# Performance work log

Measured on AMD Instinct MI355X. Metric: run time of the kernel, lower is better.

Reference implementation:

```python
import jax, jax.numpy as jnp
import numpy as np

VOCAB = 50257
EXTRA = 64          # static over-approximation of num_oovs
SEQ = 1024
T_DEC = 100
E = 128
H = 160             # encoder hidden per direction; decoder hidden = 2H = 320
UNK = 3
START = 0
NEG = -1e9


def lstm_cell(x, h, c, wih, whh, bih, bhh):
    # torch gate order: i, f, g, o
    g = x @ wih.T + h @ whh.T + bih + bhh
    i, f, gg, o = jnp.split(g, 4, axis=-1)
    c = jax.nn.sigmoid(f) * c + jax.nn.sigmoid(i) * jnp.tanh(gg)
    h = jax.nn.sigmoid(o) * jnp.tanh(c)
    return h, c


def run_lstm(xs, wih, whh, bih, bhh, hdim):
    def step(carry, x):
        h, c = carry
        h, c = lstm_cell(x, h, c, wih, whh, bih, bhh)
        return (h, c), h
    init = (jnp.zeros((hdim,), xs.dtype), jnp.zeros((hdim,), xs.dtype))
    (hf, _), hs = jax.lax.scan(step, init, xs)
    return hs, hf


def setup_inputs() -> dict:
    key = jax.random.key(0)
    ks = jax.random.split(key, 20)
    rn = lambda k, shape, s: (jax.random.normal(k, shape, dtype=jnp.float32) * s)
    inp = {
        'input_ids': jax.random.randint(ks[0], (SEQ,), 0, VOCAB + EXTRA),
        'embedding': rn(ks[1], (VOCAB, E), 0.1),
        'enc_wih_f': rn(ks[2], (4 * H, E), 0.08),
        'enc_whh_f': rn(ks[3], (4 * H, H), 0.08),
        'enc_bih_f': rn(ks[4], (4 * H,), 0.05),
        'enc_bhh_f': rn(ks[5], (4 * H,), 0.05),
        'enc_wih_b': rn(ks[6], (4 * H, E), 0.08),
        'enc_whh_b': rn(ks[7], (4 * H, H), 0.08),
        'enc_bih_b': rn(ks[8], (4 * H,), 0.05),
        'enc_bhh_b': rn(ks[9], (4 * H,), 0.05),
        'dec_wih': rn(ks[10], (8 * H, E), 0.08),
        'dec_whh': rn(ks[11], (8 * H, 2 * H), 0.08),
        'dec_bih': rn(ks[12], (8 * H,), 0.05),
        'dec_bhh': rn(ks[13], (8 * H,), 0.05),
        'enc_attn_proj': rn(ks[14], (2 * H, 2 * H), 0.02),
        'dec_attn_proj': rn(ks[15], (2 * H, 2 * H), 0.02),
        'vocab_proj': rn(ks[16], (E, 6 * H), 0.05),
        'out_bias': rn(ks[17], (VOCAB,), 0.01),
        'switch_w': rn(ks[18], (1, 6 * H), 0.05),
        'switch_b': rn(ks[19], (1,), 0.05),
    }
    return inp


def reference(input_ids, embedding, enc_wih_f, enc_whh_f, enc_bih_f, enc_bhh_f,
              enc_wih_b, enc_whh_b, enc_bih_b, enc_bhh_b,
              dec_wih, dec_whh, dec_bih, dec_bhh,
              enc_attn_proj, dec_attn_proj, vocab_proj, out_bias,
              switch_w, switch_b):
    ids_in = jnp.where(input_ids >= VOCAB, UNK, input_ids)
    emb = embedding[ids_in]                               # [S, E]

    # bidirectional encoder LSTM
    h_fwd, hfin_f = run_lstm(emb, enc_wih_f, enc_whh_f, enc_bih_f, enc_bhh_f, H)
    h_bwd_rev, hfin_b = run_lstm(emb[::-1], enc_wih_b, enc_whh_b, enc_bih_b, enc_bhh_b, H)
    enc_h = jnp.concatenate([h_fwd, h_bwd_rev[::-1]], axis=-1)   # [S, 2H]

    # step-invariant vocab projection: tanh(W_emb @ vocab_proj) -> [V, 6H]
    out_proj = jnp.tanh(embedding @ vocab_proj)

    # precompute projected encoder states for attention: [S, 2H]
    enc_proj_h = enc_h @ enc_attn_proj.T

    h0 = jnp.concatenate([hfin_f, hfin_b])                # [2H]
    c0 = jnp.zeros((2 * H,), enc_h.dtype)
    dec_buf0 = jnp.zeros((T_DEC, 2 * H), enc_h.dtype)
    cum0 = jnp.zeros((SEQ,), enc_h.dtype)
    tok0 = jnp.asarray(START, dtype=input_ids.dtype)
    t_range = jnp.arange(T_DEC)

    def step(carry, t):
        h, c, cum, dec_buf, tok = carry
        x = embedding[jnp.where(tok >= VOCAB, UNK, tok)]
        h, c = lstm_cell(x, h, c, dec_wih, dec_whh, dec_bih, dec_bhh)

        # intra-temporal encoder attention
        scores = enc_proj_h @ h                           # [S] = h @ W_e @ enc_h.T
        cum_safe = jnp.where(t == 0, 1.0, cum)
        temporal = jnp.where(t == 0, scores, jnp.exp(scores) / cum_safe)
        attn = jax.nn.softmax(temporal)
        enc_ctx = attn @ enc_h                            # [2H]

        # intra-decoder attention over previous decoder hidden states
        dscores = (h @ dec_attn_proj) @ dec_buf.T         # [T_DEC]
        dmask = t_range < t
        dattn = jax.nn.softmax(jnp.where(dmask, dscores, NEG))
        dec_ctx = jnp.where(t == 0, jnp.zeros_like(h), dattn @ dec_buf)

        concat = jnp.concatenate([h, enc_ctx, dec_ctx])   # [6H]
        vocab_dist = jax.nn.softmax(out_proj @ concat + out_bias)  # [V]
        p_copy = jax.nn.sigmoid(jnp.dot(switch_w[0], concat) + switch_b[0])
        gen = jnp.pad((1.0 - p_copy) * vocab_dist, (0, EXTRA))     # [V+EXTRA]
        final = gen.at[input_ids].add(p_copy * attn)      # pointer scatter-add

        cum = cum + scores
        dec_buf = dec_buf.at[t].set(h)
        tok = jnp.argmax(final).astype(input_ids.dtype)   # greedy decode
        return (h, c, cum, dec_buf, tok), final

    _, finals = jax.lax.scan(step, (h0, c0, cum0, dec_buf0, tok0), t_range)
    return finals                                         # [T_DEC, V+EXTRA]
```

## Files before the change

kernel.cpp:

```cpp
#include <hip/hip_runtime.h>
#include <cstdint>

#define VOCAB 50257
#define VTOT  50321
#define TDEC  100
#define UNK   3
#define VPB   99

static const size_t OFF_EMB    = 0;
static const size_t OFF_WIHT_F = 131072;
static const size_t OFF_WIHT_B = 212992;
static const size_t OFF_WTE    = 294912;
static const size_t OFF_XG     = 397312;
static const size_t OFF_ENCH   = 1708032;
static const size_t OFF_EPH    = 2035712;
static const size_t OFF_DECBUF = 2363392;
static const size_t OFF_LOGITS = 2395392;
static const size_t OFF_SCORES = 2446080;
static const size_t OFF_GATES  = 2447104;
static const size_t OFF_HPAR   = 2448384;
static const size_t OFF_CPAR   = 2450944;
static const size_t OFF_DCTX   = 2456064;
static const size_t OFF_H      = 2456384;
static const size_t OFF_H0     = 2456704;
static const size_t OFF_CA     = 2457024;
static const size_t OFF_CB     = 2457344;
static const size_t OFF_CUMA   = 2457664;
static const size_t OFF_CUMB   = 2458688;
static const size_t OFF_ATTN   = 2459712;
static const size_t OFF_BM     = 2460736;
static const size_t OFF_BS     = 2461248;
static const size_t OFF_AVAL   = 2461760;
static const size_t OFF_AIDX   = 2462272;
static const size_t OFF_SCAL   = 2462784;
static const size_t OFF_SKEY   = 2462848;
static const size_t OFF_SPOS   = 2463872;
static const size_t OFF_BSTART = 2464896;
static const size_t OFF_WBF16  = 2465792;

__device__ __forceinline__ float sigmf(float x) { return 1.f / (1.f + expf(-x)); }

__device__ __forceinline__ float wsum64(float x) {
#pragma unroll
  for (int m = 1; m < 64; m <<= 1) x += __shfl_xor(x, m, 64);
  return x;
}

__device__ __forceinline__ unsigned short bf16r(float x) {
  uint32_t b = __float_as_uint(x);
  uint32_t r = (b + 0x7fffu + ((b >> 16) & 1u)) >> 16;
  return (unsigned short)r;
}

__global__ __launch_bounds__(256) void k_setup(float* __restrict__ ws, const int* __restrict__ ids,
                                               const float* __restrict__ embt, const float* __restrict__ ewf,
                                               const float* __restrict__ ewb, const float* __restrict__ eap) {
  int idx = blockIdx.x * 256 + threadIdx.x;
  if (idx < 131072) {
    int tt = idx >> 7, e = idx & 127;
    int id = ids[tt]; if (id >= VOCAB) id = UNK;
    ws[OFF_EMB + idx] = embt[(size_t)id * 128 + e];
  } else if (idx < 212992) {
    int i = idx - 131072;
    int k = i / 640, g = i - (i / 640) * 640;
    ws[OFF_WIHT_F + i] = ewf[(size_t)g * 128 + k];
  } else if (idx < 294912) {
    int i = idx - 212992;
    int k = i / 640, g = i - (i / 640) * 640;
    ws[OFF_WIHT_B + i] = ewb[(size_t)g * 128 + k];
  } else if (idx < 397312) {
    int i = idx - 294912;
    int k = i / 320, j = i - (i / 320) * 320;
    ws[OFF_WTE + i] = eap[(size_t)j * 320 + k];
  } else if (idx < 398656) {
    int i = idx - 397312;
    if (i < 320) ws[OFF_CA + i] = 0.f;
    else         ws[OFF_CUMA + (i - 320)] = 0.f;
  }
}

__global__ __launch_bounds__(256) void k_xg(float* __restrict__ ws,
                                            const float* __restrict__ bif, const float* __restrict__ bhf,
                                            const float* __restrict__ bib, const float* __restrict__ bhb) {
  int idx = blockIdx.x * 256 + threadIdx.x;
  int d = idx / 655360;
  int r = idx - d * 655360;
  int tt = r / 640, g = r - (r / 640) * 640;
  const float* wT = ws + (d ? OFF_WIHT_B : OFF_WIHT_F);
  const float* er = ws + OFF_EMB + (size_t)(d ? (1023 - tt) : tt) * 128;
  float acc = d ? (bib[g] + bhb[g]) : (bif[g] + bhf[g]);
#pragma unroll 4
  for (int k = 0; k < 128; ++k) acc += er[k] * wT[(size_t)k * 640 + g];
  ws[OFF_XG + idx] = acc;
}

__global__ __launch_bounds__(256) void k_outproj(const float* __restrict__ embt, const float* __restrict__ vp,
                                                 float* __restrict__ ws) {
  __shared__ float As[64][128];
  __shared__ float Bs[128][64];
  const int tid = threadIdx.x;
  const int v0 = blockIdx.x * 64, n0 = blockIdx.y * 64;
  for (int c = 0; c < 32; ++c) {
    int idx = c * 256 + tid;
    int m = idx >> 7, k = idx & 127;
    int v = v0 + m;
    As[m][k] = (v < VOCAB) ? embt[(size_t)v * 128 + k] : 0.f;
    int k2 = idx >> 6, n = idx & 63;
    Bs[k2][n] = vp[(size_t)k2 * 960 + n0 + n];
  }
  __syncthreads();
  const int mi = tid >> 4, ni = tid & 15;
  float acc[4][4] = {};
  for (int k = 0; k < 128; ++k) {
    float a0 = As[mi * 4 + 0][k], a1 = As[mi * 4 + 1][k], a2 = As[mi * 4 + 2][k], a3 = As[mi * 4 + 3][k];
    float4 b = *(const float4*)&Bs[k][ni * 4];
    acc[0][0] += a0 * b.x; acc[0][1] += a0 * b.y; acc[0][2] += a0 * b.z; acc[0][3] += a0 * b.w;
    acc[1][0] += a1 * b.x; acc[1][1] += a1 * b.y; acc[1][2] += a1 * b.z; acc[1][3] += a1 * b.w;
    acc[2][0] += a2 * b.x; acc[2][1] += a2 * b.y; acc[2][2] += a2 * b.z; acc[2][3] += a2 * b.w;
    acc[3][0] += a3 * b.x; acc[3][1] += a3 * b.y; acc[3][2] += a3 * b.z; acc[3][3] += a3 * b.w;
  }
  unsigned short* W = (unsigned short*)(ws + OFF_WBF16);
#pragma unroll
  for (int i = 0; i < 4; ++i) {
    int v = v0 + mi * 4 + i;
    if (v < VOCAB) {
      ushort4 pk;
      pk.x = bf16r(tanhf(acc[i][0]));
      pk.y = bf16r(tanhf(acc[i][1]));
      pk.z = bf16r(tanhf(acc[i][2]));
      pk.w = bf16r(tanhf(acc[i][3]));
      *(ushort4*)&W[(size_t)v * 960 + n0 + ni * 4] = pk;
    }
  }
}

__global__ __launch_bounds__(512) void k_encoder(float* __restrict__ ws, const float* __restrict__ whh_f,
                                                 const float* __restrict__ whh_b) {
  const int dir = blockIdx.x;
  const int tid = threadIdx.x;
  const float* whh = dir ? whh_b : whh_f;
  const float* xg = ws + OFF_XG + (size_t)dir * 655360;
  __shared__ float hbuf[160];
  __shared__ float part[4][640];
  const int q = tid & 127, kg = tid >> 7, ks = kg * 40;
  float w[5][40];
#pragma unroll
  for (int j = 0; j < 5; ++j)
#pragma unroll
    for (int i = 0; i < 40; ++i)
      w[j][i] = whh[(size_t)(5 * q + j) * 160 + ks + i];
  float cst = 0.f;
  if (tid < 160) hbuf[tid] = 0.f;
  __syncthreads();
  for (int t = 0; t < 1024; ++t) {
    float acc[5] = {0.f, 0.f, 0.f, 0.f, 0.f};
#pragma unroll
    for (int i4 = 0; i4 < 10; ++i4) {
      float4 h4 = *(const float4*)&hbuf[ks + i4 * 4];
#pragma unroll
      for (int j = 0; j < 5; ++j)
        acc[j] += w[j][i4 * 4 + 0] * h4.x + w[j][i4 * 4 + 1] * h4.y + w[j][i4 * 4 + 2] * h4.z + w[j][i4 * 4 + 3] * h4.w;
    }
#pragma unroll
    for (int j = 0; j < 5; ++j) part[kg][5 * q + j] = acc[j];
    __syncthreads();
    if (tid < 160) {
      float gi = xg[(size_t)t * 640 + tid];
      float gf = xg[(size_t)t * 640 + 160 + tid];
      float gg = xg[(size_t)t * 640 + 320 + tid];
      float go = xg[(size_t)t * 640 + 480 + tid];
#pragma unroll
      for (int k2 = 0; k2 < 4; ++k2) {
        gi += part[k2][tid]; gf += part[k2][160 + tid];
        gg += part[k2][320 + tid]; go += part[k2][480 + tid];
      }
      cst = sigmf(gf) * cst + sigmf(gi) * tanhf(gg);
      float hn = sigmf(go) * tanhf(cst);
      hbuf[tid] = hn;
      int trow = dir ? (1023 - t) : t;
      ws[OFF_ENCH + (size_t)trow * 320 + dir * 160 + tid] = hn;
    }
    __syncthreads();
  }
  if (tid < 160) ws[OFF_H0 + dir * 160 + tid] = hbuf[tid];
}

__global__ __launch_bounds__(256) void k_encproj(float* __restrict__ ws) {
  int idx = blockIdx.x * 256 + threadIdx.x;
  int s = idx / 320, j = idx - (idx / 320) * 320;
  const float* er = ws + OFF_ENCH + (size_t)s * 320;
  const float* wt = ws + OFF_WTE;
  float acc = 0.f;
#pragma unroll 4
  for (int k = 0; k < 320; ++k) acc += er[k] * wt[(size_t)k * 320 + j];
  ws[OFF_EPH + idx] = acc;
}

__global__ __launch_bounds__(512) void k_sort(float* __restrict__ ws, const int* __restrict__ ids) {
  __shared__ int sk[1024], sp[1024];
  const int tid = threadIdx.x;
  for (int j = tid; j < 1024; j += 512) { sk[j] = ids[j]; sp[j] = j; }
  if (tid < 320) ws[OFF_H + tid] = ws[OFF_H0 + tid];
  __syncthreads();
  for (int k = 2; k <= 1024; k <<= 1)
    for (int j = k >> 1; j > 0; j >>= 1) {
      for (int i = tid; i < 1024; i += 512) {
        int ixj = i ^ j;
        if (ixj > i) {
          bool up = ((i & k) == 0);
          int a = sk[i], b2 = sk[ixj];
          if (up ? (a > b2) : (a < b2)) {
            sk[i] = b2; sk[ixj] = a;
            int pa = sp[i]; sp[i] = sp[ixj]; sp[ixj] = pa;
          }
        }
      }
      __syncthreads();
    }
  int* BST = (int*)(ws + OFF_BSTART);
  int* SK = (int*)(ws + OFF_SKEY);
  int* SP = (int*)(ws + OFF_SPOS);
  for (int j = tid; j < 1024; j += 512) {
    SK[j] = sk[j]; SP[j] = sp[j];
    int o1 = sk[j] / VPB;
    int o0 = (j == 0) ? -1 : (sk[j - 1] / VPB);
    for (int o = o0 + 1; o <= o1; ++o) BST[o] = j;
  }
  if (tid == 0) {
    int olast = sk[1023] / VPB;
    for (int o = olast + 1; o <= 512; ++o) BST[o] = 1024;
  }
}

__global__ __launch_bounds__(256) void k_d1_gates(float* __restrict__ ws, const float* __restrict__ embt,
                                                  const float* __restrict__ dwih, const float* __restrict__ dwhh,
                                                  const float* __restrict__ dbih, const float* __restrict__ dbhh,
                                                  int t) {
  __shared__ float rv[256];
  __shared__ int ri[256];
  const int tid = threadIdx.x, bid = blockIdx.x;
  int token = 0;
  if (t > 0) {
    float v0 = ws[OFF_AVAL + tid], v1 = ws[OFF_AVAL + 256 + tid];
    int i0 = ((const int*)(ws + OFF_AIDX))[tid], i1 = ((const int*)(ws + OFF_AIDX))[256 + tid];
    if (v1 > v0 || (v1 == v0 && i1 < i0)) { v0 = v1; i0 = i1; }
    rv[tid] = v0; ri[tid] = i0;
    __syncthreads();
    for (int off = 128; off > 0; off >>= 1) {
      if (tid < off) {
        float b = rv[tid + off]; int bi = ri[tid + off];
        if (b > rv[tid] || (b == rv[tid] && bi < ri[tid])) { rv[tid] = b; ri[tid] = bi; }
      }
      __syncthreads();
    }
    token = ri[0];
  }
  int tokm = (token >= VOCAB) ? UNK : token;
  const int l = tid & 63, wv = tid >> 6;
  float xv0 = embt[(size_t)tokm * 128 + l];
  float xv1 = embt[(size_t)tokm * 128 + 64 + l];
  float hv[5];
#pragma unroll
  for (int c = 0; c < 5; ++c) hv[c] = ws[OFF_H + c * 64 + l];
  const int wg = bid * 4 + wv;
  for (int i = 0; i < 16; ++i) {
    const int r = wg * 16 + i;
    float acc = dwih[(size_t)r * 128 + l] * xv0 + dwih[(size_t)r * 128 + 64 + l] * xv1;
#pragma unroll
    for (int c = 0; c < 5; ++c) acc += dwhh[(size_t)r * 320 + c * 64 + l] * hv[c];
    acc = wsum64(acc);
    if (l == 0) ws[OFF_GATES + r] = acc + dbih[r] + dbhh[r];
  }
}

__global__ __launch_bounds__(512) void k_d2_hs(float* __restrict__ ws, const float* __restrict__ dap, int t) {
  __shared__ float hL[320];
  const int tid = threadIdx.x, bid = blockIdx.x;
  const int par = t & 1;
  const float* cin = ws + (par ? OFF_CB : OFF_CA);
  float* cout = ws + (par ? OFF_CA : OFF_CB);
  if (tid < 320) {
    float gi = ws[OFF_GATES + tid];
    float gf = ws[OFF_GATES + 320 + tid];
    float gg = ws[OFF_GATES + 640 + tid];
    float go = ws[OFF_GATES + 960 + tid];
    float c = sigmf(gf) * cin[tid] + sigmf(gi) * tanhf(gg);
    float hn = sigmf(go) * tanhf(c);
    hL[tid] = hn;
    if (bid == 0) {
      cout[tid] = c;
      ws[OFF_H + tid] = hn;
      ws[OFF_DECBUF + (size_t)t * 320 + tid] = hn;
    }
  }
  __syncthreads();
  if (bid < 32) {
    const int l = tid & 63, wv = tid >> 6;
    float hv[5];
#pragma unroll
    for (int c = 0; c < 5; ++c) hv[c] = hL[c * 64 + l];
#pragma unroll
    for (int i = 0; i < 4; ++i) {
      int s = bid * 32 + wv * 4 + i;
      const float* er = ws + OFF_EPH + (size_t)s * 320;
      float acc = 0.f;
#pragma unroll
      for (int c = 0; c < 5; ++c) acc += er[c * 64 + l] * hv[c];
      acc = wsum64(acc);
      if (l == 0) ws[OFF_SCORES + s] = acc;
    }
  } else if (tid < 320) {
    int q = bid - 32;
    float acc = 0.f;
#pragma unroll 8
    for (int ii = 0; ii < 40; ++ii) {
      int i = q * 40 + ii;
      acc += hL[i] * dap[(size_t)i * 320 + tid];
    }
    ws[OFF_HPAR + q * 320 + tid] = acc;
  }
}

__global__ __launch_bounds__(512) void k_d3_attn(float* __restrict__ ws, int t) {
  __shared__ float attnL[1024];
  __shared__ float redA[512];
  __shared__ float dsL[128];
  __shared__ float daL[128];
  __shared__ float hpL[320];
  const int tid = threadIdx.x, bid = blockIdx.x;
  const int par = t & 1;
  const float* cumin = ws + (par ? OFF_CUMB : OFF_CUMA);
  float* cumout = ws + (par ? OFF_CUMA : OFF_CUMB);

  if (bid < 16) {
    float s0 = ws[OFF_SCORES + tid];
    float s1 = ws[OFF_SCORES + 512 + tid];
    float t0 = (t == 0) ? s0 : expf(s0) / cumin[tid];
    float t1 = (t == 0) ? s1 : expf(s1) / cumin[512 + tid];
    redA[tid] = fmaxf(t0, t1);
    __syncthreads();
    for (int off = 256; off > 0; off >>= 1) { if (tid < off) redA[tid] = fmaxf(redA[tid], redA[tid + off]); __syncthreads(); }
    float mx = redA[0];
    __syncthreads();
    redA[tid] = expf(t0 - mx) + expf(t1 - mx);
    __syncthreads();
    for (int off = 256; off > 0; off >>= 1) { if (tid < off) redA[tid] += redA[tid + off]; __syncthreads(); }
    float Ssm = redA[0];
    __syncthreads();
    attnL[tid] = expf(t0 - mx) / Ssm;
    attnL[512 + tid] = expf(t1 - mx) / Ssm;
    __syncthreads();
    if (tid < 64) ws[OFF_ATTN + bid * 64 + tid] = attnL[bid * 64 + tid];
    if (tid < 320) {
      float acc = 0.f;
      const float* eh = ws + OFF_ENCH + (size_t)(bid * 64) * 320 + tid;
#pragma unroll 4
      for (int k2 = 0; k2 < 64; ++k2) acc += attnL[bid * 64 + k2] * eh[(size_t)k2 * 320];
      ws[OFF_CPAR + bid * 320 + tid] = acc;
    }
  } else {
    cumout[tid] = cumin[tid] + ws[OFF_SCORES + tid];
    cumout[512 + tid] = cumin[512 + tid] + ws[OFF_SCORES + 512 + tid];
    if (tid < 320) {
      float a = 0.f;
#pragma unroll
      for (int q = 0; q < 8; ++q) a += ws[OFF_HPAR + q * 320 + tid];
      hpL[tid] = a;
    }
    __syncthreads();
    const int l = tid & 63, wv = tid >> 6;
    float hpv[5];
#pragma unroll
    for (int c = 0; c < 5; ++c) hpv[c] = hpL[c * 64 + l];
#pragma unroll
    for (int k2 = 0; k2 < 13; ++k2) {
      int tp = wv + 8 * k2;
      if (tp < t) {
        float acc = 0.f;
#pragma unroll
        for (int c = 0; c < 5; ++c) acc += hpv[c] * ws[OFF_DECBUF + (size_t)tp * 320 + c * 64 + l];
        acc = wsum64(acc);
        if (l == 0) dsL[tp] = acc;
      }
    }
    __syncthreads();
    float dv = -1e30f;
    if (tid < 128) { dv = (tid < t) ? dsL[tid] : -1e30f; redA[tid] = dv; }
    __syncthreads();
    for (int off = 64; off > 0; off >>= 1) { if (tid < off) redA[tid] = fmaxf(redA[tid], redA[tid + off]); __syncthreads(); }
    float dmx = redA[0];
    __syncthreads();
    float de = (tid < 128) ? expf(dv - dmx) : 0.f;
    if (tid < 128) redA[tid] = de;
    __syncthreads();
    for (int off = 64; off > 0; off >>= 1) { if (tid < off) redA[tid] += redA[tid + off]; __syncthreads(); }
    float dS = redA[0];
    __syncthreads();
    if (tid < 128) daL[tid] = de / dS;
    __syncthreads();
    if (tid < 320) {
      float acc = 0.f;
      for (int tp = 0; tp < t; ++tp) acc += daL[tp] * ws[OFF_DECBUF + (size_t)tp * 320 + tid];
      ws[OFF_DCTX + tid] = acc;
    }
  }
}

__global__ __launch_bounds__(256) void k_d4_logits(float* __restrict__ ws, const float* __restrict__ ob,
                                                   const float* __restrict__ sw, const float* __restrict__ sb) {
  __shared__ float concatL[960];
  __shared__ float logitsL[128];
  __shared__ float rm[256], rs[256];
  const int tid = threadIdx.x, bid = blockIdx.x;
  for (int i = tid; i < 960; i += 256) {
    float v;
    if (i < 320) v = ws[OFF_H + i];
    else if (i < 640) {
      int j = i - 320;
      float a = 0.f;
#pragma unroll
      for (int p = 0; p < 16; ++p) a += ws[OFF_CPAR + p * 320 + j];
      v = a;
    } else v = ws[OFF_DCTX + (i - 640)];
    concatL[i] = v;
  }
  __syncthreads();
  const int l = tid & 63, wv = tid >> 6;
  if (bid == 0 && tid < 64) {
    float acc = 0.f;
#pragma unroll
    for (int c = 0; c < 15; ++c) acc += sw[c * 64 + l] * concatL[c * 64 + l];
    acc = wsum64(acc);
    if (l == 0) ws[OFF_SCAL] = 1.f / (1.f + expf(-(acc + sb[0])));
  }
  const unsigned* W = (const unsigned*)(ws + OFF_WBF16);
  const float2* cL2 = (const float2*)concatL;
  float cc0[7], cc1[7], ct0 = 0.f, ct1 = 0.f;
#pragma unroll
  for (int c = 0; c < 7; ++c) { float2 x = cL2[c * 64 + l]; cc0[c] = x.x; cc1[c] = x.y; }
  if (l < 32) { ct0 = concatL[896 + 2 * l]; ct1 = concatL[897 + 2 * l]; }
  const int vbase = bid * VPB;
  const int r0 = wv * 25, r1 = (wv * 25 + 25 < VPB) ? (wv * 25 + 25) : VPB;
  for (int r = r0; r < r1; r += 2) {
    int va = vbase + r, vb = va + 1;
    bool oka = (va < VOCAB);
    bool okb = (r + 1 < r1) && (vb < VOCAB);
    float acc0 = 0.f, acc1 = 0.f;
    const unsigned* rowa = W + (size_t)va * 480;
    const unsigned* rowb = W + (size_t)vb * 480;
    unsigned ua[7], ub[7], ta = 0, tb = 0;
    if (oka) {
#pragma unroll
      for (int c = 0; c < 7; ++c) ua[c] = rowa[c * 64 + l];
      if (l < 32) ta = rowa[448 + l];
    }
    if (okb) {
#pragma unroll
      for (int c = 0; c < 7; ++c) ub[c] = rowb[c * 64 + l];
      if (l < 32) tb = rowb[448 + l];
    }
    if (oka) {
#pragma unroll
      for (int c = 0; c < 7; ++c)
        acc0 += __uint_as_float(ua[c] << 16) * cc0[c] + __uint_as_float(ua[c] & 0xffff0000u) * cc1[c];
      if (l < 32) acc0 += __uint_as_float(ta << 16) * ct0 + __uint_as_float(ta & 0xffff0000u) * ct1;
    }
    if (okb) {
#pragma unroll
      for (int c = 0; c < 7; ++c)
        acc1 += __uint_as_float(ub[c] << 16) * cc0[c] + __uint_as_float(ub[c] & 0xffff0000u) * cc1[c];
      if (l < 32) acc1 += __uint_as_float(tb << 16) * ct0 + __uint_as_float(tb & 0xffff0000u) * ct1;
    }
    acc0 = wsum64(acc0);
    acc1 = wsum64(acc1);
    if (l == 0) {
      if (oka) { float lg = acc0 + ob[va]; logitsL[r] = lg; ws[OFF_LOGITS + va] = lg; }
      else logitsL[r] = -1e30f;
      if (r + 1 < r1) {
        if (okb) { float lg = acc1 + ob[vb]; logitsL[r + 1] = lg; ws[OFF_LOGITS + vb] = lg; }
        else logitsL[r + 1] = -1e30f;
      }
    }
  }
  __syncthreads();
  bool valid = (tid < VPB) && (logitsL[tid < VPB ? tid : 0] > -1e29f) && (tid < VPB);
  float m = -1e30f, s = 0.f;
  if (tid < VPB) {
    float lv = logitsL[tid];
    if (lv > -1e29f) { m = lv; s = 1.f; }
  }
  (void)valid;
  rm[tid] = m; rs[tid] = s;
  __syncthreads();
  for (int off = 128; off > 0; off >>= 1) {
    if (tid < off) {
      float m1 = rm[tid], m2 = rm[tid + off];
      float mm = fmaxf(m1, m2);
      rs[tid] = rs[tid] * expf(m1 - mm) + rs[tid + off] * expf(m2 - mm);
      rm[tid] = mm;
    }
    __syncthreads();
  }
  if (tid == 0) { ws[OFF_BM + bid] = rm[0]; ws[OFF_BS + bid] = rs[0]; }
}

__global__ __launch_bounds__(128) void k_d5_final(float* __restrict__ ws, float* __restrict__ out, int t) {
  __shared__ float rm[128], rs[128];
  __shared__ float rv[128];
  __shared__ int ri[128];
  const int tid = threadIdx.x, bid = blockIdx.x;
  float m = -1e30f, s = 0.f;
#pragma unroll
  for (int k = 0; k < 4; ++k) {
    float m2 = ws[OFF_BM + tid * 4 + k], s2 = ws[OFF_BS + tid * 4 + k];
    float mm = fmaxf(m, m2);
    s = s * expf(m - mm) + s2 * expf(m2 - mm);
    m = mm;
  }
  rm[tid] = m; rs[tid] = s;
  __syncthreads();
  for (int off = 64; off > 0; off >>= 1) {
    if (tid < off) {
      float m1 = rm[tid], m2 = rm[tid + off];
      float mm = fmaxf(m1, m2);
      rs[tid] = rs[tid] * expf(m1 - mm) + rs[tid + off] * expf(m2 - mm);
      rm[tid] = mm;
    }
    __syncthreads();
  }
  float M = rm[0], Sg = rs[0];
  float pc = ws[OFF_SCAL];
  float scale = (1.f - pc) / Sg;
  const int* BST = (const int*)(ws + OFF_BSTART);
  const int* SK = (const int*)(ws + OFF_SKEY);
  const int* SP = (const int*)(ws + OFF_SPOS);
  int v = bid * VPB + tid;
  bool act = (tid < VPB) && (v < VTOT);
  float val = -1e30f;
  if (act) {
    val = (v < VOCAB) ? scale * expf(ws[OFF_LOGITS + v] - M) : 0.f;
    int jb = BST[bid], je = BST[bid + 1];
    for (int j = jb; j < je; ++j)
      if (SK[j] == v) val += pc * ws[OFF_ATTN + SP[j]];
    out[(size_t)t * VTOT + v] = val;
  }
  rv[tid] = act ? val : -1e30f; ri[tid] = v;
  __syncthreads();
  for (int off = 64; off > 0; off >>= 1) {
    if (tid < off) {
      float v2 = rv[tid + off]; int i2 = ri[tid + off];
      if (v2 > rv[tid] || (v2 == rv[tid] && i2 < ri[tid])) { rv[tid] = v2; ri[tid] = i2; }
    }
    __syncthreads();
  }
  if (tid == 0) { ws[OFF_AVAL + bid] = rv[0]; ((int*)(ws + OFF_AIDX))[bid] = ri[0]; }
}

extern "C" void kernel_launch(void* const* d_in, const int* in_sizes, int n_in,
                              void* d_out, int out_size, void* d_ws, size_t ws_size,
                              hipStream_t stream) {
  const int*   ids  = (const int*)d_in[0];
  const float* embt = (const float*)d_in[1];
  const float* ewf  = (const float*)d_in[2];
  const float* ehf  = (const float*)d_in[3];
  const float* ebif = (const float*)d_in[4];
  const float* ebhf = (const float*)d_in[5];
  const float* ewb  = (const float*)d_in[6];
  const float* ehb  = (const float*)d_in[7];
  const float* ebib = (const float*)d_in[8];
  const float* ebhb = (const float*)d_in[9];
  const float* dwih = (const float*)d_in[10];
  const float* dwhh = (const float*)d_in[11];
  const float* dbih = (const float*)d_in[12];
  const float* dbhh = (const float*)d_in[13];
  const float* eap  = (const float*)d_in[14];
  const float* dap  = (const float*)d_in[15];
  const float* vp   = (const float*)d_in[16];
  const float* ob   = (const float*)d_in[17];
  const float* sw   = (const float*)d_in[18];
  const float* sb   = (const float*)d_in[19];
  float* out = (float*)d_out;
  float* ws  = (float*)d_ws;

  k_setup<<<1558, 256, 0, stream>>>(ws, ids, embt, ewf, ewb, eap);
  k_xg<<<5120, 256, 0, stream>>>(ws, ebif, ebhf, ebib, ebhb);
  k_outproj<<<dim3(786, 15), 256, 0, stream>>>(embt, vp, ws);
  k_encoder<<<2, 512, 0, stream>>>(ws, ehf, ehb);
  k_encproj<<<1280, 256, 0, stream>>>(ws);
  k_sort<<<1, 512, 0, stream>>>(ws, ids);

  for (int t = 0; t < TDEC; ++t) {
    k_d1_gates<<<20, 256, 0, stream>>>(ws, embt, dwih, dwhh, dbih, dbhh, t);
    k_d2_hs<<<40, 512, 0, stream>>>(ws, dap, t);
    k_d3_attn<<<17, 512, 0, stream>>>(ws, t);
    k_d4_logits<<<512, 256, 0, stream>>>(ws, ob, sw, sb);
    k_d5_final<<<512, 128, 0, stream>>>(ws, out, t);
  }
}
```

Before: 7.844 ms.

## Run encoder recurrence concurrently with output projection; vectorize logits row loads

Merges the serial encoder LSTM (2 blocks) and the vocab output-projection GEMM into one launch, so the long sequential encoder runs alongside the GEMM tiles instead of after them. The encoder projection and the id sort are likewise merged into one launch. The per-step logits kernel now has each lane load two 16-byte bf16 chunks of a row with contiguous 16-element concat slices, replacing strided 4-byte loads. The GEMM tiles move to 512 threads with a padded A tile, and the scheduling of the two encoder blocks relative to the many GEMM blocks is not guaranteed.

```diff
diff --git a/kernel.cpp b/kernel.cpp
--- a/kernel.cpp
+++ b/kernel.cpp
@@ -52,6 +52,9 @@
   return (unsigned short)r;
 }
 
+__device__ __forceinline__ float bflo(unsigned u) { return __uint_as_float(u << 16); }
+__device__ __forceinline__ float bfhi(unsigned u) { return __uint_as_float(u & 0xffff0000u); }
+
 __global__ __launch_bounds__(256) void k_setup(float* __restrict__ ws, const int* __restrict__ ids,
                                                const float* __restrict__ embt, const float* __restrict__ ewf,
                                                const float* __restrict__ ewb, const float* __restrict__ eap) {
@@ -94,141 +97,147 @@
   ws[OFF_XG + idx] = acc;
 }
 
-__global__ __launch_bounds__(256) void k_outproj(const float* __restrict__ embt, const float* __restrict__ vp,
-                                                 float* __restrict__ ws) {
-  __shared__ float As[64][128];
-  __shared__ float Bs[128][64];
-  const int tid = threadIdx.x;
-  const int v0 = blockIdx.x * 64, n0 = blockIdx.y * 64;
-  for (int c = 0; c < 32; ++c) {
-    int idx = c * 256 + tid;
-    int m = idx >> 7, k = idx & 127;
-    int v = v0 + m;
-    As[m][k] = (v < VOCAB) ? embt[(size_t)v * 128 + k] : 0.f;
-    int k2 = idx >> 6, n = idx & 63;
-    Bs[k2][n] = vp[(size_t)k2 * 960 + n0 + n];
-  }
-  __syncthreads();
-  const int mi = tid >> 4, ni = tid & 15;
-  float acc[4][4] = {};
-  for (int k = 0; k < 128; ++k) {
-    float a0 = As[mi * 4 + 0][k], a1 = As[mi * 4 + 1][k], a2 = As[mi * 4 + 2][k], a3 = As[mi * 4 + 3][k];
-    float4 b = *(const float4*)&Bs[k][ni * 4];
-    acc[0][0] += a0 * b.x; acc[0][1] += a0 * b.y; acc[0][2] += a0 * b.z; acc[0][3] += a0 * b.w;
-    acc[1][0] += a1 * b.x; acc[1][1] += a1 * b.y; acc[1][2] += a1 * b.z; acc[1][3] += a1 * b.w;
-    acc[2][0] += a2 * b.x; acc[2][1] += a2 * b.y; acc[2][2] += a2 * b.z; acc[2][3] += a2 * b.w;
-    acc[3][0] += a3 * b.x; acc[3][1] += a3 * b.y; acc[3][2] += a3 * b.z; acc[3][3] += a3 * b.w;
-  }
-  unsigned short* W = (unsigned short*)(ws + OFF_WBF16);
-#pragma unroll
-  for (int i = 0; i < 4; ++i) {
-    int v = v0 + mi * 4 + i;
-    if (v < VOCAB) {
-      ushort4 pk;
-      pk.x = bf16r(tanhf(acc[i][0]));
-      pk.y = bf16r(tanhf(acc[i][1]));
-      pk.z = bf16r(tanhf(acc[i][2]));
-      pk.w = bf16r(tanhf(acc[i][3]));
-      *(ushort4*)&W[(size_t)v * 960 + n0 + ni * 4] = pk;
-    }
-  }
-}
-
-__global__ __launch_bounds__(512) void k_encoder(float* __restrict__ ws, const float* __restrict__ whh_f,
-                                                 const float* __restrict__ whh_b) {
-  const int dir = blockIdx.x;
-  const int tid = threadIdx.x;
-  const float* whh = dir ? whh_b : whh_f;
-  const float* xg = ws + OFF_XG + (size_t)dir * 655360;
-  __shared__ float hbuf[160];
-  __shared__ float part[4][640];
-  const int q = tid & 127, kg = tid >> 7, ks = kg * 40;
-  float w[5][40];
-#pragma unroll
-  for (int j = 0; j < 5; ++j)
-#pragma unroll
-    for (int i = 0; i < 40; ++i)
-      w[j][i] = whh[(size_t)(5 * q + j) * 160 + ks + i];
-  float cst = 0.f;
-  if (tid < 160) hbuf[tid] = 0.f;
-  __syncthreads();
-  for (int t = 0; t < 1024; ++t) {
-    float acc[5] = {0.f, 0.f, 0.f, 0.f, 0.f};
-#pragma unroll
-    for (int i4 = 0; i4 < 10; ++i4) {
-      float4 h4 = *(const float4*)&hbuf[ks + i4 * 4];
-#pragma unroll
-      for (int j = 0; j < 5; ++j)
-        acc[j] += w[j][i4 * 4 + 0] * h4.x + w[j][i4 * 4 + 1] * h4.y + w[j][i4 * 4 + 2] * h4.z + w[j][i4 * 4 + 3] * h4.w;
-    }
-#pragma unroll
-    for (int j = 0; j < 5; ++j) part[kg][5 * q + j] = acc[j];
-    __syncthreads();
-    if (tid < 160) {
-      float gi = xg[(size_t)t * 640 + tid];
-      float gf = xg[(size_t)t * 640 + 160 + tid];
-      float gg = xg[(size_t)t * 640 + 320 + tid];
-      float go = xg[(size_t)t * 640 + 480 + tid];
-#pragma unroll
-      for (int k2 = 0; k2 < 4; ++k2) {
-        gi += part[k2][tid]; gf += part[k2][160 + tid];
-        gg += part[k2][320 + tid]; go += part[k2][480 + tid];
-      }
-      cst = sigmf(gf) * cst + sigmf(gi) * tanhf(gg);
-      float hn = sigmf(go) * tanhf(cst);
-      hbuf[tid] = hn;
-      int trow = dir ? (1023 - t) : t;
-      ws[OFF_ENCH + (size_t)trow * 320 + dir * 160 + tid] = hn;
-    }
-    __syncthreads();
-  }
-  if (tid < 160) ws[OFF_H0 + dir * 160 + tid] = hbuf[tid];
-}
-
-__global__ __launch_bounds__(256) void k_encproj(float* __restrict__ ws) {
-  int idx = blockIdx.x * 256 + threadIdx.x;
-  int s = idx / 320, j = idx - (idx / 320) * 320;
-  const float* er = ws + OFF_ENCH + (size_t)s * 320;
-  const float* wt = ws + OFF_WTE;
-  float acc = 0.f;
+__global__ __launch_bounds__(512) void k_encproj_fused(float* __restrict__ ws, const float* __restrict__ whh_f,
+                                                       const float* __restrict__ whh_b,
+                                                       const float* __restrict__ embt,
+                                                       const float* __restrict__ vp) {
+  __shared__ float POOL[12352];
+  const int tid = threadIdx.x, bid = blockIdx.x;
+  if (bid < 2) {
+    const int dir = bid;
+    const float* whh = dir ? whh_b : whh_f;
+    const float* xg = ws + OFF_XG + (size_t)dir * 655360;
+    float* hbuf = POOL;
+    float* part = POOL + 160;
+    const int q = tid & 127, kg = tid >> 7, ks = kg * 40;
+    float w[5][40];
+#pragma unroll
+    for (int j = 0; j < 5; ++j)
+#pragma unroll
+      for (int i = 0; i < 40; ++i)
+        w[j][i] = whh[(size_t)(5 * q + j) * 160 + ks + i];
+    float cst = 0.f;
+    if (tid < 160) hbuf[tid] = 0.f;
+    __syncthreads();
+    for (int t = 0; t < 1024; ++t) {
+      float acc[5] = {0.f, 0.f, 0.f, 0.f, 0.f};
+#pragma unroll
+      for (int i4 = 0; i4 < 10; ++i4) {
+        float4 h4 = *(const float4*)&hbuf[ks + i4 * 4];
+#pragma unroll
+        for (int j = 0; j < 5; ++j)
+          acc[j] += w[j][i4 * 4 + 0] * h4.x + w[j][i4 * 4 + 1] * h4.y + w[j][i4 * 4 + 2] * h4.z + w[j][i4 * 4 + 3] * h4.w;
+      }
+#pragma unroll
+      for (int j = 0; j < 5; ++j) part[kg * 640 + 5 * q + j] = acc[j];
+      __syncthreads();
+      if (tid < 160) {
+        float gi = xg[(size_t)t * 640 + tid];
+        float gf = xg[(size_t)t * 640 + 160 + tid];
+        float gg = xg[(size_t)t * 640 + 320 + tid];
+        float go = xg[(size_t)t * 640 + 480 + tid];
+#pragma unroll
+        for (int k2 = 0; k2 < 4; ++k2) {
+          gi += part[k2 * 640 + tid]; gf += part[k2 * 640 + 160 + tid];
+          gg += part[k2 * 640 + 320 + tid]; go += part[k2 * 640 + 480 + tid];
+        }
+        cst = sigmf(gf) * cst + sigmf(gi) * tanhf(gg);
+        float hn = sigmf(go) * tanhf(cst);
+        hbuf[tid] = hn;
+        int trow = dir ? (1023 - t) : t;
+        ws[OFF_ENCH + (size_t)trow * 320 + dir * 160 + tid] = hn;
+      }
+      __syncthreads();
+    }
+    if (tid < 160) ws[OFF_H0 + dir * 160 + tid] = hbuf[tid];
+  } else {
+    float* As = POOL;
+    float* Bs = POOL + 8256;
+    unsigned short* Wo = (unsigned short*)(ws + OFF_WBF16);
+    const int mi = tid >> 4, ni = tid & 15;
+    const int tile = bid - 2;
+    int v0 = (tile % 786) * 64, n0 = (tile / 786) * 64;
+#pragma unroll
+    for (int c = 0; c < 16; ++c) {
+      int idx = c * 512 + tid;
+      int m = idx >> 7, k = idx & 127;
+      As[m * 129 + k] = (v0 + m < VOCAB) ? embt[(size_t)(v0 + m) * 128 + k] : 0.f;
+    }
+    float acc[2][4] = {};
+    for (int half = 0; half < 2; ++half) {
+      __syncthreads();
+#pragma unroll
+      for (int c = 0; c < 8; ++c) {
+        int idx = c * 512 + tid;
+        int k = idx >> 6, n = idx & 63;
+        Bs[k * 64 + n] = vp[(size_t)(half * 64 + k) * 960 + n0 + n];
+      }
+      __syncthreads();
+      for (int k = 0; k < 64; ++k) {
+        float a0 = As[(mi * 2) * 129 + half * 64 + k];
+        float a1 = As[(mi * 2 + 1) * 129 + half * 64 + k];
+        float4 b = *(const float4*)&Bs[k * 64 + ni * 4];
+        acc[0][0] += a0 * b.x; acc[0][1] += a0 * b.y; acc[0][2] += a0 * b.z; acc[0][3] += a0 * b.w;
+        acc[1][0] += a1 * b.x; acc[1][1] += a1 * b.y; acc[1][2] += a1 * b.z; acc[1][3] += a1 * b.w;
+      }
+    }
+#pragma unroll
+    for (int i = 0; i < 2; ++i) {
+      int v = v0 + mi * 2 + i;
+      if (v < VOCAB) {
+        ushort4 pk;
+        pk.x = bf16r(tanhf(acc[i][0])); pk.y = bf16r(tanhf(acc[i][1]));
+        pk.z = bf16r(tanhf(acc[i][2])); pk.w = bf16r(tanhf(acc[i][3]));
+        *(ushort4*)&Wo[(size_t)v * 960 + n0 + ni * 4] = pk;
+      }
+    }
+  }
+}
+
+__global__ __launch_bounds__(512) void k_encproj_sort(float* __restrict__ ws, const int* __restrict__ ids) {
+  const int tid = threadIdx.x, bid = blockIdx.x;
+  if (bid < 640) {
+    int idx = bid * 512 + tid;
+    int s = idx / 320, j = idx - (idx / 320) * 320;
+    const float* er = ws + OFF_ENCH + (size_t)s * 320;
+    const float* wt = ws + OFF_WTE;
+    float acc = 0.f;
 #pragma unroll 4
-  for (int k = 0; k < 320; ++k) acc += er[k] * wt[(size_t)k * 320 + j];
-  ws[OFF_EPH + idx] = acc;
-}
-
-__global__ __launch_bounds__(512) void k_sort(float* __restrict__ ws, const int* __restrict__ ids) {
-  __shared__ int sk[1024], sp[1024];
-  const int tid = threadIdx.x;
-  for (int j = tid; j < 1024; j += 512) { sk[j] = ids[j]; sp[j] = j; }
-  if (tid < 320) ws[OFF_H + tid] = ws[OFF_H0 + tid];
-  __syncthreads();
-  for (int k = 2; k <= 1024; k <<= 1)
-    for (int j = k >> 1; j > 0; j >>= 1) {
-      for (int i = tid; i < 1024; i += 512) {
-        int ixj = i ^ j;
-        if (ixj > i) {
-          bool up = ((i & k) == 0);
-          int a = sk[i], b2 = sk[ixj];
-          if (up ? (a > b2) : (a < b2)) {
-            sk[i] = b2; sk[ixj] = a;
-            int pa = sp[i]; sp[i] = sp[ixj]; sp[ixj] = pa;
+    for (int k = 0; k < 320; ++k) acc += er[k] * wt[(size_t)k * 320 + j];
+    ws[OFF_EPH + idx] = acc;
+  } else {
+    __shared__ int sk[1024], sp[1024];
+    for (int j = tid; j < 1024; j += 512) { sk[j] = ids[j]; sp[j] = j; }
+    if (tid < 320) ws[OFF_H + tid] = ws[OFF_H0 + tid];
+    __syncthreads();
+    for (int k = 2; k <= 1024; k <<= 1)
+      for (int j = k >> 1; j > 0; j >>= 1) {
+        for (int i = tid; i < 1024; i += 512) {
+          int ixj = i ^ j;
+          if (ixj > i) {
+            bool up = ((i & k) == 0);
+            int a = sk[i], b2 = sk[ixj];
+            if (up ? (a > b2) : (a < b2)) {
+              sk[i] = b2; sk[ixj] = a;
+              int pa = sp[i]; sp[i] = sp[ixj]; sp[ixj] = pa;
+            }
           }
         }
-      }
-      __syncthreads();
-    }
-  int* BST = (int*)(ws + OFF_BSTART);
-  int* SK = (int*)(ws + OFF_SKEY);
-  int* SP = (int*)(ws + OFF_SPOS);
-  for (int j = tid; j < 1024; j += 512) {
-    SK[j] = sk[j]; SP[j] = sp[j];
-    int o1 = sk[j] / VPB;
-    int o0 = (j == 0) ? -1 : (sk[j - 1] / VPB);
-    for (int o = o0 + 1; o <= o1; ++o) BST[o] = j;
-  }
-  if (tid == 0) {
-    int olast = sk[1023] / VPB;
-    for (int o = olast + 1; o <= 512; ++o) BST[o] = 1024;
+        __syncthreads();
+      }
+    int* BST = (int*)(ws + OFF_BSTART);
+    int* SK = (int*)(ws + OFF_SKEY);
+    int* SP = (int*)(ws + OFF_SPOS);
+    for (int j = tid; j < 1024; j += 512) {
+      SK[j] = sk[j]; SP[j] = sp[j];
+      int o1 = sk[j] / VPB;
+      int o0 = (j == 0) ? -1 : (sk[j - 1] / VPB);
+      for (int o = o0 + 1; o <= o1; ++o) BST[o] = j;
+    }
+    if (tid == 0) {
+      int olast = sk[1023] / VPB;
+      for (int o = olast + 1; o <= 512; ++o) BST[o] = 1024;
+    }
   }
 }
 
@@ -433,63 +442,47 @@
     acc = wsum64(acc);
     if (l == 0) ws[OFF_SCAL] = 1.f / (1.f + expf(-(acc + sb[0])));
   }
-  const unsigned* W = (const unsigned*)(ws + OFF_WBF16);
-  const float2* cL2 = (const float2*)concatL;
-  float cc0[7], cc1[7], ct0 = 0.f, ct1 = 0.f;
-#pragma unroll
-  for (int c = 0; c < 7; ++c) { float2 x = cL2[c * 64 + l]; cc0[c] = x.x; cc1[c] = x.y; }
-  if (l < 32) { ct0 = concatL[896 + 2 * l]; ct1 = concatL[897 + 2 * l]; }
+  float cf[16];
+  if (l < 60) {
+#pragma unroll
+    for (int c = 0; c < 16; ++c) cf[c] = concatL[16 * l + c];
+  } else {
+#pragma unroll
+    for (int c = 0; c < 16; ++c) cf[c] = 0.f;
+  }
+  const uint4* W4 = (const uint4*)((const unsigned*)(ws + OFF_WBF16));
   const int vbase = bid * VPB;
   const int r0 = wv * 25, r1 = (wv * 25 + 25 < VPB) ? (wv * 25 + 25) : VPB;
-  for (int r = r0; r < r1; r += 2) {
-    int va = vbase + r, vb = va + 1;
-    bool oka = (va < VOCAB);
-    bool okb = (r + 1 < r1) && (vb < VOCAB);
-    float acc0 = 0.f, acc1 = 0.f;
-    const unsigned* rowa = W + (size_t)va * 480;
-    const unsigned* rowb = W + (size_t)vb * 480;
-    unsigned ua[7], ub[7], ta = 0, tb = 0;
-    if (oka) {
-#pragma unroll
-      for (int c = 0; c < 7; ++c) ua[c] = rowa[c * 64 + l];
-      if (l < 32) ta = rowa[448 + l];
-    }
-    if (okb) {
-#pragma unroll
-      for (int c = 0; c < 7; ++c) ub[c] = rowb[c * 64 + l];
-      if (l < 32) tb = rowb[448 + l];
-    }
-    if (oka) {
-#pragma unroll
-      for (int c = 0; c < 7; ++c)
-        acc0 += __uint_as_float(ua[c] << 16) * cc0[c] + __uint_as_float(ua[c] & 0xffff0000u) * cc1[c];
-      if (l < 32) acc0 += __uint_as_float(ta << 16) * ct0 + __uint_as_float(ta & 0xffff0000u) * ct1;
-    }
-    if (okb) {
-#pragma unroll
-      for (int c = 0; c < 7; ++c)
-        acc1 += __uint_as_float(ub[c] << 16) * cc0[c] + __uint_as_float(ub[c] & 0xffff0000u) * cc1[c];
-      if (l < 32) acc1 += __uint_as_float(tb << 16) * ct0 + __uint_as_float(tb & 0xffff0000u) * ct1;
-    }
-    acc0 = wsum64(acc0);
-    acc1 = wsum64(acc1);
-    if (l == 0) {
-      if (oka) { float lg = acc0 + ob[va]; logitsL[r] = lg; ws[OFF_LOGITS + va] = lg; }
-      else logitsL[r] = -1e30f;
-      if (r + 1 < r1) {
-        if (okb) { float lg = acc1 + ob[vb]; logitsL[r + 1] = lg; ws[OFF_LOGITS + vb] = lg; }
-        else logitsL[r + 1] = -1e30f;
-      }
+#pragma unroll 2
+  for (int r = r0; r < r1; ++r) {
+    int v = vbase + r;
+    if (v < VOCAB) {
+      float acc = 0.f;
+      if (l < 60) {
+        const uint4* row = W4 + (size_t)v * 120;
+        uint4 a = row[2 * l];
+        uint4 b = row[2 * l + 1];
+        acc += bflo(a.x) * cf[0]  + bfhi(a.x) * cf[1]
+             + bflo(a.y) * cf[2]  + bfhi(a.y) * cf[3]
+             + bflo(a.z) * cf[4]  + bfhi(a.z) * cf[5]
+             + bflo(a.w) * cf[6]  + bfhi(a.w) * cf[7]
+             + bflo(b.x) * cf[8]  + bfhi(b.x) * cf[9]
+             + bflo(b.y) * cf[10] + bfhi(b.y) * cf[11]
+             + bflo(b.z) * cf[12] + bfhi(b.z) * cf[13]
+             + bflo(b.w) * cf[14] + bfhi(b.w) * cf[15];
+      }
+      acc = wsum64(acc);
+      if (l == 0) { float lg = acc + ob[v]; logitsL[r] = lg; ws[OFF_LOGITS + v] = lg; }
+    } else if (l == 0) {
+      logitsL[r] = -1e30f;
     }
   }
   __syncthreads();
-  bool valid = (tid < VPB) && (logitsL[tid < VPB ? tid : 0] > -1e29f) && (tid < VPB);
   float m = -1e30f, s = 0.f;
   if (tid < VPB) {
     float lv = logitsL[tid];
     if (lv > -1e29f) { m = lv; s = 1.f; }
   }
-  (void)valid;
   rm[tid] = m; rs[tid] = s;
   __syncthreads();
   for (int off = 128; off > 0; off >>= 1) {
@@ -584,10 +577,8 @@
 
   k_setup<<<1558, 256, 0, stream>>>(ws, ids, embt, ewf, ewb, eap);
   k_xg<<<5120, 256, 0, stream>>>(ws, ebif, ebhf, ebib, ebhb);
-  k_outproj<<<dim3(786, 15), 256, 0, stream>>>(embt, vp, ws);
-  k_encoder<<<2, 512, 0, stream>>>(ws, ehf, ehb);
-  k_encproj<<<1280, 256, 0, stream>>>(ws);
-  k_sort<<<1, 512, 0, stream>>>(ws, ids);
+  k_encproj_fused<<<786 * 15 + 2, 512, 0, stream>>>(ws, ehf, ehb, embt, vp);
+  k_encproj_sort<<<641, 512, 0, stream>>>(ws, ids);
 
   for (int t = 0; t < TDEC; ++t) {
     k_d1_gates<<<20, 256, 0, stream>>>(ws, embt, dwih, dwhh, dbih, dbhh, t);
```

After: 23.51 ms. 200% more time.

## Fuse decoder hidden-state/score kernel with attention kernel, recomputing scores per block

Applied to the files above, without the earlier changes.

Merges the hidden-state update plus encoder-score kernel with the attention kernel into one 17-block launch. Each block now recomputes all 1024 encoder attention scores and the full softmax redundantly in shared memory, and the last block computes the decoder attention projection serially instead of across 8 blocks. This removes one kernel launch per decode step and a global-memory round trip for scores and partial projections. In exchange each block does far more serial work: 32 iterations over the 1024x320 projected encoder matrix, and one block does the whole 320x320 matvec.

```diff
diff --git a/kernel.cpp b/kernel.cpp
--- a/kernel.cpp
+++ b/kernel.cpp
@@ -273,12 +273,21 @@
   }
 }
 
-__global__ __launch_bounds__(512) void k_d2_hs(float* __restrict__ ws, const float* __restrict__ dap, int t) {
+__global__ __launch_bounds__(512) void k_d23(float* __restrict__ ws, const float* __restrict__ dap, int t) {
+  __shared__ float scoresL[1024];
+  __shared__ float attnL[1024];
+  __shared__ float redA[512];
+  __shared__ float dsL[128];
+  __shared__ float daL[128];
   __shared__ float hL[320];
+  __shared__ float hpL[320];
   const int tid = threadIdx.x, bid = blockIdx.x;
   const int par = t & 1;
   const float* cin = ws + (par ? OFF_CB : OFF_CA);
   float* cout = ws + (par ? OFF_CA : OFF_CB);
+  const float* cumin = ws + (par ? OFF_CUMB : OFF_CUMA);
+  float* cumout = ws + (par ? OFF_CUMA : OFF_CUMB);
+
   if (tid < 320) {
     float gi = ws[OFF_GATES + tid];
     float gf = ws[OFF_GATES + 320 + tid];
@@ -294,62 +303,43 @@
     }
   }
   __syncthreads();
-  if (bid < 32) {
+  {
     const int l = tid & 63, wv = tid >> 6;
     float hv[5];
 #pragma unroll
     for (int c = 0; c < 5; ++c) hv[c] = hL[c * 64 + l];
-#pragma unroll
-    for (int i = 0; i < 4; ++i) {
-      int s = bid * 32 + wv * 4 + i;
-      const float* er = ws + OFF_EPH + (size_t)s * 320;
-      float acc = 0.f;
-#pragma unroll
-      for (int c = 0; c < 5; ++c) acc += er[c * 64 + l] * hv[c];
-      acc = wsum64(acc);
-      if (l == 0) ws[OFF_SCORES + s] = acc;
-    }
-  } else if (tid < 320) {
-    int q = bid - 32;
-    float acc = 0.f;
-#pragma unroll 8
-    for (int ii = 0; ii < 40; ++ii) {
-      int i = q * 40 + ii;
-      acc += hL[i] * dap[(size_t)i * 320 + tid];
-    }
-    ws[OFF_HPAR + q * 320 + tid] = acc;
-  }
-}
-
-__global__ __launch_bounds__(512) void k_d3_attn(float* __restrict__ ws, int t) {
-  __shared__ float attnL[1024];
-  __shared__ float redA[512];
-  __shared__ float dsL[128];
-  __shared__ float daL[128];
-  __shared__ float hpL[320];
-  const int tid = threadIdx.x, bid = blockIdx.x;
-  const int par = t & 1;
-  const float* cumin = ws + (par ? OFF_CUMB : OFF_CUMA);
-  float* cumout = ws + (par ? OFF_CUMA : OFF_CUMB);
+    for (int j = 0; j < 32; ++j) {
+#pragma unroll
+      for (int i = 0; i < 4; ++i) {
+        int s = j * 32 + wv * 4 + i;
+        const float* er = ws + OFF_EPH + (size_t)s * 320;
+        float acc = 0.f;
+#pragma unroll
+        for (int c = 0; c < 5; ++c) acc += er[c * 64 + l] * hv[c];
+        acc = wsum64(acc);
+        if (l == 0) scoresL[s] = acc;
+      }
+    }
+  }
+  __syncthreads();
+  float s0 = scoresL[tid], s1 = scoresL[512 + tid];
+  float t0 = (t == 0) ? s0 : expf(s0) / cumin[tid];
+  float t1 = (t == 0) ? s1 : expf(s1) / cumin[512 + tid];
+  redA[tid] = fmaxf(t0, t1);
+  __syncthreads();
+  for (int off = 256; off > 0; off >>= 1) { if (tid < off) redA[tid] = fmaxf(redA[tid], redA[tid + off]); __syncthreads(); }
+  float mx = redA[0];
+  __syncthreads();
+  redA[tid] = expf(t0 - mx) + expf(t1 - mx);
+  __syncthreads();
+  for (int off = 256; off > 0; off >>= 1) { if (tid < off) redA[tid] += redA[tid + off]; __syncthreads(); }
+  float Ssm = redA[0];
+  __syncthreads();
+  attnL[tid] = expf(t0 - mx) / Ssm;
+  attnL[512 + tid] = expf(t1 - mx) / Ssm;
+  __syncthreads();
 
   if (bid < 16) {
-    float s0 = ws[OFF_SCORES + tid];
-    float s1 = ws[OFF_SCORES + 512 + tid];
-    float t0 = (t == 0) ? s0 : expf(s0) / cumin[tid];
-    float t1 = (t == 0) ? s1 : expf(s1) / cumin[512 + tid];
-    redA[tid] = fmaxf(t0, t1);
-    __syncthreads();
-    for (int off = 256; off > 0; off >>= 1) { if (tid < off) redA[tid] = fmaxf(redA[tid], redA[tid + off]); __syncthreads(); }
-    float mx = redA[0];
-    __syncthreads();
-    redA[tid] = expf(t0 - mx) + expf(t1 - mx);
-    __syncthreads();
-    for (int off = 256; off > 0; off >>= 1) { if (tid < off) redA[tid] += redA[tid + off]; __syncthreads(); }
-    float Ssm = redA[0];
-    __syncthreads();
-    attnL[tid] = expf(t0 - mx) / Ssm;
-    attnL[512 + tid] = expf(t1 - mx) / Ssm;
-    __syncthreads();
     if (tid < 64) ws[OFF_ATTN + bid * 64 + tid] = attnL[bid * 64 + tid];
     if (tid < 320) {
       float acc = 0.f;
@@ -359,12 +349,20 @@
       ws[OFF_CPAR + bid * 320 + tid] = acc;
     }
   } else {
-    cumout[tid] = cumin[tid] + ws[OFF_SCORES + tid];
-    cumout[512 + tid] = cumin[512 + tid] + ws[OFF_SCORES + 512 + tid];
+    cumout[tid] = cumin[tid] + scoresL[tid];
+    cumout[512 + tid] = cumin[512 + tid] + scoresL[512 + tid];
     if (tid < 320) {
       float a = 0.f;
 #pragma unroll
-      for (int q = 0; q < 8; ++q) a += ws[OFF_HPAR + q * 320 + tid];
+      for (int q = 0; q < 8; ++q) {
+        float pq = 0.f;
+#pragma unroll 8
+        for (int ii = 0; ii < 40; ++ii) {
+          int i = q * 40 + ii;
+          pq += hL[i] * dap[(size_t)i * 320 + tid];
+        }
+        a += pq;
+      }
       hpL[tid] = a;
     }
     __syncthreads();
@@ -483,13 +481,11 @@
     }
   }
   __syncthreads();
-  bool valid = (tid < VPB) && (logitsL[tid < VPB ? tid : 0] > -1e29f) && (tid < VPB);
   float m = -1e30f, s = 0.f;
   if (tid < VPB) {
     float lv = logitsL[tid];
     if (lv > -1e29f) { m = lv; s = 1.f; }
   }
-  (void)valid;
   rm[tid] = m; rs[tid] = s;
   __syncthreads();
   for (int off = 128; off > 0; off >>= 1) {
@@ -591,8 +587,7 @@
 
   for (int t = 0; t < TDEC; ++t) {
     k_d1_gates<<<20, 256, 0, stream>>>(ws, embt, dwih, dwhh, dbih, dbhh, t);
-    k_d2_hs<<<40, 512, 0, stream>>>(ws, dap, t);
-    k_d3_attn<<<17, 512, 0, stream>>>(ws, t);
+    k_d23<<<17, 512, 0, stream>>>(ws, dap, t);
     k_d4_logits<<<512, 256, 0, stream>>>(ws, ob, sw, sb);
     k_d5_final<<<512, 128, 0, stream>>>(ws, out, t);
   }
```

After: 14.98 ms. 1.91x slower.
